# Optimization experiments

Hardware: AMD Instinct MI355X
Metric: run time of the kernel (lower is better)

## Reference

```python
import jax, jax.numpy as jnp
import numpy as np

BSZ, D = 64, 65536
N_NODES, N_FEATS, EMBED_DIM = 1024, 256, 256


def setup_inputs() -> dict:
    key = jax.random.key(0)
    k1, k2, k3, k4, k5, k6 = jax.random.split(key, 6)
    flat_inputs = jax.random.normal(k1, (BSZ, D), dtype=jnp.float32)
    node_ids = jax.random.randint(k2, (BSZ, D), 0, N_NODES, dtype=jnp.int64 if jax.config.jax_enable_x64 else jnp.int32)
    feat_ids = jax.random.randint(k3, (BSZ, D), 0, N_FEATS, dtype=jnp.int64 if jax.config.jax_enable_x64 else jnp.int32)
    # Linear(n_feats -> embed_dim): W is (embed_dim, n_feats) like torch, plus bias.
    lim = 1.0 / np.sqrt(N_FEATS)
    W = jax.random.uniform(k4, (EMBED_DIM, N_FEATS), minval=-lim, maxval=lim, dtype=jnp.float32)
    b = jax.random.uniform(k5, (EMBED_DIM,), minval=-lim, maxval=lim, dtype=jnp.float32)
    global_emb = jax.random.normal(k6, (N_NODES, EMBED_DIM), dtype=jnp.float32)
    return {"flat_inputs": flat_inputs, "node_ids": node_ids, "feat_ids": feat_ids,
            "W": W, "b": b, "global_emb": global_emb}


def _expand(vals, node_ids, feat_ids, n_nodes, n_feats):
    # scatter-fill a dense (bsz, n_nodes, n_feats) tensor (zeros elsewhere)
    bsz, d = vals.shape
    batch_ids = jnp.broadcast_to(jnp.arange(bsz)[:, None], (bsz, d))
    out = jnp.zeros((bsz, n_nodes, n_feats), dtype=vals.dtype)
    return out.at[batch_ids.ravel(), node_ids.ravel(), feat_ids.ravel()].set(vals.ravel())


def reference(flat_inputs, node_ids, feat_ids, W, b, global_emb):
    obs_mat = _expand(flat_inputs, node_ids, feat_ids, N_NODES, N_FEATS)
    mask_mat = _expand(jnp.ones_like(flat_inputs), node_ids, feat_ids, N_NODES, N_FEATS)
    obs_counts = mask_mat.sum(-1, keepdims=True)            # (bsz, n_nodes, 1)
    obs_masked = jnp.nan_to_num((obs_mat * mask_mat) / obs_counts)
    missing_node_mask = obs_counts == 0
    # nodewise Linear + global embedding broadcast over batch
    embedded = jnp.einsum('bnf,ef->bne', obs_masked, W) + b + global_emb[None, :, :]
    return embedded, missing_node_mask
```

## Files before the change

### kernel.cpp

```cpp
#include <hip/hip_runtime.h>
#include <hip/hip_bf16.h>

#define BSZ    64
#define DLEN   65536
#define NNODES 1024
#define NFEATS 256
#define EDIM   256
#define NROWS  (BSZ * NNODES)

#define NRANGE  16
#define NBUCKET (BSZ * NRANGE)
#define LCAP    320
#define GCAP    4600
#define WPAD    268

typedef __bf16 bf16x8 __attribute__((ext_vector_type(8)));
typedef float  f32x4  __attribute__((ext_vector_type(4)));

__device__ __forceinline__ unsigned short f2bf(float x) {
  union { float f; unsigned u; } c; c.f = x;
  unsigned r = c.u + 0x7FFFu + ((c.u >> 16) & 1u);
  return (unsigned short)(r >> 16);
}

__global__ __launch_bounds__(256) void wconv_kernel(
    const float* __restrict__ W, unsigned short* __restrict__ Wb,
    unsigned* __restrict__ gcnt) {
  int i = (blockIdx.x * 256 + threadIdx.x) * 4;
  float4 w = *(const float4*)(W + i);
  ushort4 o;
  o.x = f2bf(w.x); o.y = f2bf(w.y); o.z = f2bf(w.z); o.w = f2bf(w.w);
  *(ushort4*)(Wb + i) = o;
  if (blockIdx.x == 0) ((uint4*)gcnt)[threadIdx.x] = make_uint4(0u, 0u, 0u, 0u);
}

__global__ __launch_bounds__(512, 6) void bucket_kernel(
    const float* __restrict__ x, const int* __restrict__ nid,
    const int* __restrict__ fid, unsigned* __restrict__ gcnt,
    uint2* __restrict__ gbuf) {
  __shared__ uint2 lbuf[NRANGE][LCAP];
  __shared__ unsigned lcnt[NRANGE];
  __shared__ unsigned lbase[NRANGE];

  const int t = threadIdx.x;
  if (t < NRANGE) lcnt[t] = 0;
  __syncthreads();

  const int b = blockIdx.x >> 4;
  const int base = blockIdx.x * 4096;

#pragma unroll
  for (int k = 0; k < 2; ++k) {
    int i = base + (k * 512 + t) * 4;
    float4 xv = *(const float4*)(x + i);
    int4   nv = *(const int4*)(nid + i);
    int4   fv = *(const int4*)(fid + i);
    int   nd[4] = {nv.x, nv.y, nv.z, nv.w};
    int   ft[4] = {fv.x, fv.y, fv.z, fv.w};
    float vl[4] = {xv.x, xv.y, xv.z, xv.w};
#pragma unroll
    for (int j = 0; j < 4; ++j) {
      int d = (i + j) & 0xFFFF;
      unsigned pack = (((unsigned)(d + 1)) << 15) | ((unsigned)f2bf(vl[j]) >> 1);
      int r = nd[j] >> 6;
      unsigned row = (unsigned)(nd[j] & 63);
      uint2 rec;
      rec.x = pack;
      rec.y = (row << 16) | (row * WPAD + (unsigned)ft[j]);
      unsigned li = atomicAdd(&lcnt[r], 1u);
      if (li < LCAP) {
        lbuf[r][li] = rec;
      } else {
        unsigned gi = atomicAdd(&gcnt[b * NRANGE + r], 1u);
        if (gi < GCAP) gbuf[(size_t)(b * NRANGE + r) * GCAP + gi] = rec;
      }
    }
  }
  __syncthreads();

  if (t < NRANGE) {
    unsigned n = lcnt[t]; if (n > LCAP) n = LCAP;
    lcnt[t] = n;
    lbase[t] = atomicAdd(&gcnt[b * NRANGE + t], n);
  }
  __syncthreads();

  for (int r = 0; r < NRANGE; ++r) {
    unsigned n  = lcnt[r];
    unsigned bs = lbase[r];
    uint2* dst = gbuf + (size_t)(b * NRANGE + r) * GCAP;
    for (unsigned j = t; j < n; j += 512) {
      unsigned gi = bs + j;
      if (gi < GCAP) dst[gi] = lbuf[r][j];
    }
  }
}

__global__ __launch_bounds__(512, 4) void fused_kernel(
    const unsigned* __restrict__ gcnt, const uint2* __restrict__ gbuf,
    const unsigned short* __restrict__ Wb, const float* __restrict__ bias,
    const float* __restrict__ gemb,
    float* __restrict__ out_emb, float* __restrict__ out_mask) {
  __shared__ __align__(16) unsigned win[64 * WPAD];
  __shared__ int counts[64];
  __shared__ float scl[64];

  const int t = threadIdx.x;
  const int g = blockIdx.x;
  const int row0 = g * 64;
  const int nb = (g & 15) * 64;

  uint4* wz = (uint4*)win;
  for (int j = t; j < (64 * WPAD) / 4; j += 512) wz[j] = make_uint4(0u, 0u, 0u, 0u);
  if (t < 64) counts[t] = 0;
  __syncthreads();

  int cn = (int)gcnt[g]; if (cn > GCAP) cn = GCAP;
  const uint2* bk = gbuf + (size_t)g * GCAP;
  const uint4* bk4 = (const uint4*)bk;
  int np = cn >> 1;
  for (int j = t; j < np; j += 512) {
    uint4 rr = bk4[j];
    unsigned old0 = atomicMax(&win[rr.y & 0xFFFFu], rr.x);
    if (old0 == 0u) atomicAdd(&counts[rr.y >> 16], 1);
    unsigned old1 = atomicMax(&win[rr.w & 0xFFFFu], rr.z);
    if (old1 == 0u) atomicAdd(&counts[rr.w >> 16], 1);
  }
  if ((cn & 1) && t == 0) {
    uint2 rec = bk[cn - 1];
    unsigned old = atomicMax(&win[rec.y & 0xFFFFu], rec.x);
    if (old == 0u) atomicAdd(&counts[rec.y >> 16], 1);
  }
  __syncthreads();

  if (t < 64) {
    int c = counts[t];
    scl[t] = c ? 1.0f / (float)c : 0.0f;
    out_mask[row0 + t] = c ? 0.0f : 1.0f;
  }

  const int wv   = t >> 6;
  const int lane = t & 63;
  const int cl   = lane & 15;
  const int q    = lane >> 4;
  const int col0 = wv * 32;

  f32x4 acc[4][2];
#pragma unroll
  for (int mt = 0; mt < 4; ++mt)
#pragma unroll
    for (int nt = 0; nt < 2; ++nt) acc[mt][nt] = (f32x4)(0.0f);

#pragma unroll
  for (int ks = 0; ks < 8; ++ks) {
    bf16x8 bfr[2];
#pragma unroll
    for (int nt = 0; nt < 2; ++nt) {
      const uint4* wp = (const uint4*)(Wb + (size_t)(col0 + nt * 16 + cl) * NFEATS + ks * 32 + q * 8);
      bfr[nt] = __builtin_bit_cast(bf16x8, *wp);
    }
#pragma unroll
    for (int mt = 0; mt < 4; ++mt) {
      const uint4* ap = (const uint4*)&win[(mt * 16 + cl) * WPAD + ks * 32 + q * 8];
      uint4 lo = ap[0], hi = ap[1];
      uint4 pk;
      pk.x = ((lo.x & 0x7FFFu) << 1) | ((lo.y & 0x7FFFu) << 17);
      pk.y = ((lo.z & 0x7FFFu) << 1) | ((lo.w & 0x7FFFu) << 17);
      pk.z = ((hi.x & 0x7FFFu) << 1) | ((hi.y & 0x7FFFu) << 17);
      pk.w = ((hi.z & 0x7FFFu) << 1) | ((hi.w & 0x7FFFu) << 17);
      bf16x8 afr = __builtin_bit_cast(bf16x8, pk);
#pragma unroll
      for (int nt = 0; nt < 2; ++nt)
        acc[mt][nt] = __builtin_amdgcn_mfma_f32_16x16x32_bf16(afr, bfr[nt], acc[mt][nt], 0, 0, 0);
    }
  }
  __syncthreads();

#pragma unroll
  for (int nt = 0; nt < 2; ++nt) {
    int col = col0 + nt * 16 + cl;
    float bv = bias[col];
#pragma unroll
    for (int mt = 0; mt < 4; ++mt) {
#pragma unroll
      for (int r2 = 0; r2 < 4; ++r2) {
        int row = mt * 16 + q * 4 + r2;
        float o = acc[mt][nt][r2] * scl[row] + bv + gemb[(size_t)(nb + row) * EDIM + col];
        out_emb[(size_t)(row0 + row) * EDIM + col] = o;
      }
    }
  }
}

extern "C" void kernel_launch(void* const* d_in, const int* in_sizes, int n_in,
                              void* d_out, int out_size, void* d_ws, size_t ws_size,
                              hipStream_t stream) {
  const float* x    = (const float*)d_in[0];
  const int*   nid  = (const int*)d_in[1];
  const int*   fid  = (const int*)d_in[2];
  const float* W    = (const float*)d_in[3];
  const float* bias = (const float*)d_in[4];
  const float* gemb = (const float*)d_in[5];

  float* out_emb  = (float*)d_out;
  float* out_mask = out_emb + (size_t)NROWS * EDIM;

  unsigned* gcnt = (unsigned*)d_ws;
  uint2* gbuf = (uint2*)((char*)d_ws + 8192);
  unsigned short* Wb = (unsigned short*)((char*)d_ws + 8192 + (size_t)NBUCKET * GCAP * sizeof(uint2));

  wconv_kernel<<<64, 256, 0, stream>>>(W, Wb, gcnt);
  bucket_kernel<<<(BSZ * DLEN) / 4096, 512, 0, stream>>>(x, nid, fid, gcnt, gbuf);
  fused_kernel<<<NBUCKET, 512, 0, stream>>>(gcnt, gbuf, Wb, bias, gemb, out_emb, out_mask);
}
```

Baseline: 148.7 us.

## Split each bucket's 64-row tile across two blocks and count occupancy by scanning

Each fused block now handles half of a bucket's 64 node rows, so twice as many smaller blocks launch with half the shared-memory window, and the occupancy hint rises to allow more blocks per CU. Both halves read the full bucket record list and filter by row bit, which doubles global reads of the bucket buffer and the filtering work. Per-row counts are no longer kept with atomics. They are recomputed by scanning the window for nonzero entries with a segmented shuffle reduction. The aim is more parallelism and occupancy for the scatter and MFMA phases.

```diff
diff --git a/kernel.cpp b/kernel.cpp
--- a/kernel.cpp
+++ b/kernel.cpp
@@ -13,6 +13,7 @@
 #define LCAP    320
 #define GCAP    4600
 #define WPAD    268
+#define HROWS   32
 
 typedef __bf16 bf16x8 __attribute__((ext_vector_type(8)));
 typedef float  f32x4  __attribute__((ext_vector_type(4)));
@@ -96,47 +97,58 @@
   }
 }
 
-__global__ __launch_bounds__(512, 4) void fused_kernel(
+__global__ __launch_bounds__(512, 8) void fused_kernel(
     const unsigned* __restrict__ gcnt, const uint2* __restrict__ gbuf,
     const unsigned short* __restrict__ Wb, const float* __restrict__ bias,
     const float* __restrict__ gemb,
     float* __restrict__ out_emb, float* __restrict__ out_mask) {
-  __shared__ __align__(16) unsigned win[64 * WPAD];
-  __shared__ int counts[64];
-  __shared__ float scl[64];
+  __shared__ __align__(16) unsigned win[HROWS * WPAD];
+  __shared__ float scl[HROWS];
 
   const int t = threadIdx.x;
-  const int g = blockIdx.x;
-  const int row0 = g * 64;
-  const int nb = (g & 15) * 64;
+  const int g = blockIdx.x >> 1;
+  const int h = blockIdx.x & 1;
+  const int row0 = g * 64 + h * HROWS;
+  const int nb = (g & 15) * 64 + h * HROWS;
 
   uint4* wz = (uint4*)win;
-  for (int j = t; j < (64 * WPAD) / 4; j += 512) wz[j] = make_uint4(0u, 0u, 0u, 0u);
-  if (t < 64) counts[t] = 0;
+  for (int j = t; j < (HROWS * WPAD) / 4; j += 512) wz[j] = make_uint4(0u, 0u, 0u, 0u);
   __syncthreads();
 
   int cn = (int)gcnt[g]; if (cn > GCAP) cn = GCAP;
   const uint2* bk = gbuf + (size_t)g * GCAP;
   const uint4* bk4 = (const uint4*)bk;
+  const unsigned sub = (unsigned)(h * HROWS * WPAD);
   int np = cn >> 1;
   for (int j = t; j < np; j += 512) {
     uint4 rr = bk4[j];
-    unsigned old0 = atomicMax(&win[rr.y & 0xFFFFu], rr.x);
-    if (old0 == 0u) atomicAdd(&counts[rr.y >> 16], 1);
-    unsigned old1 = atomicMax(&win[rr.w & 0xFFFFu], rr.z);
-    if (old1 == 0u) atomicAdd(&counts[rr.w >> 16], 1);
+    if (((rr.y >> 21) & 1u) == (unsigned)h) atomicMax(&win[(rr.y & 0xFFFFu) - sub], rr.x);
+    if (((rr.w >> 21) & 1u) == (unsigned)h) atomicMax(&win[(rr.w & 0xFFFFu) - sub], rr.z);
   }
   if ((cn & 1) && t == 0) {
     uint2 rec = bk[cn - 1];
-    unsigned old = atomicMax(&win[rec.y & 0xFFFFu], rec.x);
-    if (old == 0u) atomicAdd(&counts[rec.y >> 16], 1);
-  }
-  __syncthreads();
-
-  if (t < 64) {
-    int c = counts[t];
-    scl[t] = c ? 1.0f / (float)c : 0.0f;
-    out_mask[row0 + t] = c ? 0.0f : 1.0f;
+    if (((rec.y >> 21) & 1u) == (unsigned)h) atomicMax(&win[(rec.y & 0xFFFFu) - sub], rec.x);
+  }
+  __syncthreads();
+
+  {
+    const int lr  = t >> 4;
+    const int seg = t & 15;
+    const uint4* rowp = (const uint4*)&win[lr * WPAD];
+    int c = 0;
+#pragma unroll
+    for (int j = 0; j < 4; ++j) {
+      uint4 w = rowp[seg + 16 * j];
+      c += (w.x != 0u) + (w.y != 0u) + (w.z != 0u) + (w.w != 0u);
+    }
+    c += __shfl_down(c, 8, 16);
+    c += __shfl_down(c, 4, 16);
+    c += __shfl_down(c, 2, 16);
+    c += __shfl_down(c, 1, 16);
+    if (seg == 0) {
+      scl[lr] = c ? 1.0f / (float)c : 0.0f;
+      out_mask[row0 + lr] = c ? 0.0f : 1.0f;
+    }
   }
 
   const int wv   = t >> 6;
@@ -145,9 +157,9 @@
   const int q    = lane >> 4;
   const int col0 = wv * 32;
 
-  f32x4 acc[4][2];
-#pragma unroll
-  for (int mt = 0; mt < 4; ++mt)
+  f32x4 acc[2][2];
+#pragma unroll
+  for (int mt = 0; mt < 2; ++mt)
 #pragma unroll
     for (int nt = 0; nt < 2; ++nt) acc[mt][nt] = (f32x4)(0.0f);
 
@@ -160,7 +172,7 @@
       bfr[nt] = __builtin_bit_cast(bf16x8, *wp);
     }
 #pragma unroll
-    for (int mt = 0; mt < 4; ++mt) {
+    for (int mt = 0; mt < 2; ++mt) {
       const uint4* ap = (const uint4*)&win[(mt * 16 + cl) * WPAD + ks * 32 + q * 8];
       uint4 lo = ap[0], hi = ap[1];
       uint4 pk;
@@ -181,7 +193,7 @@
     int col = col0 + nt * 16 + cl;
     float bv = bias[col];
 #pragma unroll
-    for (int mt = 0; mt < 4; ++mt) {
+    for (int mt = 0; mt < 2; ++mt) {
 #pragma unroll
       for (int r2 = 0; r2 < 4; ++r2) {
         int row = mt * 16 + q * 4 + r2;
@@ -211,5 +223,5 @@
 
   wconv_kernel<<<64, 256, 0, stream>>>(W, Wb, gcnt);
   bucket_kernel<<<(BSZ * DLEN) / 4096, 512, 0, stream>>>(x, nid, fid, gcnt, gbuf);
-  fused_kernel<<<NBUCKET, 512, 0, stream>>>(gcnt, gbuf, Wb, bias, gemb, out_emb, out_mask);
-}
+  fused_kernel<<<NBUCKET * 2, 512, 0, stream>>>(gcnt, gbuf, Wb, bias, gemb, out_emb, out_mask);
+}
```

Result: slower. 167.6 us (+12.7%).

## Fold W conversion into bucket kernel and count nonzeros after scatter

Applied to the files above, without the earlier changes.

Removes the separate weight-conversion kernel: the bf16 conversion of W now runs inside the first 32 blocks of the bucket kernel, and the counter reset becomes a memset. In the fused kernel, the per-row observed-count atomics are replaced by a post-scatter scan of the shared window that counts nonzero entries with a shuffle reduction. The record loads are also batched up front (five per thread) so they can be in flight before the atomicMax writes. The bucket kernel's occupancy hint is raised as well. The fixed five-load unroll caps each bucket at 2560 record pairs, which covers GCAP=4600 records.

```diff
diff --git a/kernel.cpp b/kernel.cpp
--- a/kernel.cpp
+++ b/kernel.cpp
@@ -23,27 +23,25 @@
   return (unsigned short)(r >> 16);
 }
 
-__global__ __launch_bounds__(256) void wconv_kernel(
-    const float* __restrict__ W, unsigned short* __restrict__ Wb,
-    unsigned* __restrict__ gcnt) {
-  int i = (blockIdx.x * 256 + threadIdx.x) * 4;
-  float4 w = *(const float4*)(W + i);
-  ushort4 o;
-  o.x = f2bf(w.x); o.y = f2bf(w.y); o.z = f2bf(w.z); o.w = f2bf(w.w);
-  *(ushort4*)(Wb + i) = o;
-  if (blockIdx.x == 0) ((uint4*)gcnt)[threadIdx.x] = make_uint4(0u, 0u, 0u, 0u);
-}
-
-__global__ __launch_bounds__(512, 6) void bucket_kernel(
+__global__ __launch_bounds__(512, 8) void bucket_kernel(
     const float* __restrict__ x, const int* __restrict__ nid,
     const int* __restrict__ fid, unsigned* __restrict__ gcnt,
-    uint2* __restrict__ gbuf) {
+    uint2* __restrict__ gbuf,
+    const float* __restrict__ W, unsigned short* __restrict__ Wb) {
   __shared__ uint2 lbuf[NRANGE][LCAP];
   __shared__ unsigned lcnt[NRANGE];
   __shared__ unsigned lbase[NRANGE];
 
   const int t = threadIdx.x;
   if (t < NRANGE) lcnt[t] = 0;
+
+  if (blockIdx.x < 32) {
+    int wi = (blockIdx.x * 512 + t) * 4;
+    float4 w = *(const float4*)(W + wi);
+    ushort4 o;
+    o.x = f2bf(w.x); o.y = f2bf(w.y); o.z = f2bf(w.z); o.w = f2bf(w.w);
+    *(ushort4*)(Wb + wi) = o;
+  }
   __syncthreads();
 
   const int b = blockIdx.x >> 4;
@@ -102,7 +100,6 @@
     const float* __restrict__ gemb,
     float* __restrict__ out_emb, float* __restrict__ out_mask) {
   __shared__ __align__(16) unsigned win[64 * WPAD];
-  __shared__ int counts[64];
   __shared__ float scl[64];
 
   const int t = threadIdx.x;
@@ -112,31 +109,50 @@
 
   uint4* wz = (uint4*)win;
   for (int j = t; j < (64 * WPAD) / 4; j += 512) wz[j] = make_uint4(0u, 0u, 0u, 0u);
-  if (t < 64) counts[t] = 0;
   __syncthreads();
 
   int cn = (int)gcnt[g]; if (cn > GCAP) cn = GCAP;
   const uint2* bk = gbuf + (size_t)g * GCAP;
   const uint4* bk4 = (const uint4*)bk;
   int np = cn >> 1;
-  for (int j = t; j < np; j += 512) {
-    uint4 rr = bk4[j];
-    unsigned old0 = atomicMax(&win[rr.y & 0xFFFFu], rr.x);
-    if (old0 == 0u) atomicAdd(&counts[rr.y >> 16], 1);
-    unsigned old1 = atomicMax(&win[rr.w & 0xFFFFu], rr.z);
-    if (old1 == 0u) atomicAdd(&counts[rr.w >> 16], 1);
-  }
-  if ((cn & 1) && t == 0) {
-    uint2 rec = bk[cn - 1];
-    unsigned old = atomicMax(&win[rec.y & 0xFFFFu], rec.x);
-    if (old == 0u) atomicAdd(&counts[rec.y >> 16], 1);
-  }
-  __syncthreads();
-
-  if (t < 64) {
-    int c = counts[t];
-    scl[t] = c ? 1.0f / (float)c : 0.0f;
-    out_mask[row0 + t] = c ? 0.0f : 1.0f;
+  {
+    uint4 r0, r1, r2, r3, r4;
+    bool v0 = t < np, v1 = t + 512 < np, v2 = t + 1024 < np,
+         v3 = t + 1536 < np, v4 = t + 2048 < np;
+    if (v0) r0 = bk4[t];
+    if (v1) r1 = bk4[t + 512];
+    if (v2) r2 = bk4[t + 1024];
+    if (v3) r3 = bk4[t + 1536];
+    if (v4) r4 = bk4[t + 2048];
+    if (v0) { atomicMax(&win[r0.y & 0xFFFFu], r0.x); atomicMax(&win[r0.w & 0xFFFFu], r0.z); }
+    if (v1) { atomicMax(&win[r1.y & 0xFFFFu], r1.x); atomicMax(&win[r1.w & 0xFFFFu], r1.z); }
+    if (v2) { atomicMax(&win[r2.y & 0xFFFFu], r2.x); atomicMax(&win[r2.w & 0xFFFFu], r2.z); }
+    if (v3) { atomicMax(&win[r3.y & 0xFFFFu], r3.x); atomicMax(&win[r3.w & 0xFFFFu], r3.z); }
+    if (v4) { atomicMax(&win[r4.y & 0xFFFFu], r4.x); atomicMax(&win[r4.w & 0xFFFFu], r4.z); }
+    if ((cn & 1) && t == 0) {
+      uint2 rec = bk[cn - 1];
+      atomicMax(&win[rec.y & 0xFFFFu], rec.x);
+    }
+  }
+  __syncthreads();
+
+  {
+    const int lr  = t >> 3;
+    const int seg = t & 7;
+    const uint4* rowp = (const uint4*)&win[lr * WPAD];
+    int c = 0;
+#pragma unroll
+    for (int j = 0; j < 8; ++j) {
+      uint4 w = rowp[seg + 8 * j];
+      c += (w.x != 0u) + (w.y != 0u) + (w.z != 0u) + (w.w != 0u);
+    }
+    c += __shfl_down(c, 4, 8);
+    c += __shfl_down(c, 2, 8);
+    c += __shfl_down(c, 1, 8);
+    if (seg == 0) {
+      scl[lr] = c ? 1.0f / (float)c : 0.0f;
+      out_mask[row0 + lr] = c ? 0.0f : 1.0f;
+    }
   }
 
   const int wv   = t >> 6;
@@ -209,7 +225,7 @@
   uint2* gbuf = (uint2*)((char*)d_ws + 8192);
   unsigned short* Wb = (unsigned short*)((char*)d_ws + 8192 + (size_t)NBUCKET * GCAP * sizeof(uint2));
 
-  wconv_kernel<<<64, 256, 0, stream>>>(W, Wb, gcnt);
-  bucket_kernel<<<(BSZ * DLEN) / 4096, 512, 0, stream>>>(x, nid, fid, gcnt, gbuf);
+  hipMemsetAsync(gcnt, 0, NBUCKET * sizeof(unsigned), stream);
+  bucket_kernel<<<(BSZ * DLEN) / 4096, 512, 0, stream>>>(x, nid, fid, gcnt, gbuf, W, Wb);
   fused_kernel<<<NBUCKET, 512, 0, stream>>>(gcnt, gbuf, Wb, bias, gemb, out_emb, out_mask);
 }
```

Result: no change. 148.3 us (-0.3%).
